# Optimization experiments

Measured on AMD Instinct MI355X. Metric: run time of the kernel, lower is better.

## Reference

```python
import jax, jax.numpy as jnp
import numpy as np

N, E, IN_FEATS, HID, CLS, K = 100000, 3200000, 500, 64, 40, 10
EPS = 1e-8

def _col_normalize(x):
    # column-wise L2 norm over nodes (dim=0), clamped at 1e-8
    return x / jnp.clip(jnp.linalg.norm(x, axis=0), EPS, None)

def setup_inputs() -> dict:
    key = jax.random.key(0)
    ks = jax.random.split(key, 9)
    features = jax.random.normal(ks[0], (N, IN_FEATS), jnp.float32)
    noise = jax.random.normal(ks[1], (N, HID), jnp.float32)
    edge_index = jax.random.randint(ks[2], (2, E), 0, N, dtype=jnp.int32)
    norm_A = jax.random.uniform(ks[3], (E,), jnp.float32) * 0.1  # normalized adj weights
    W1 = jax.random.normal(ks[4], (IN_FEATS, HID), jnp.float32) * (1.0 / np.sqrt(IN_FEATS))
    b1 = jax.random.normal(ks[5], (HID,), jnp.float32) * 0.01
    W2 = jax.random.normal(ks[6], (HID, CLS), jnp.float32) * (1.0 / np.sqrt(HID))
    b2 = jax.random.normal(ks[7], (CLS,), jnp.float32) * 0.01
    alpha = jax.random.normal(ks[8], (HID, K + 1), jnp.float32) * 0.1
    return {"features": features, "noise": noise, "norm_A": norm_A, "W1": W1,
            "b1": b1, "W2": W2, "b2": b2, "alpha": alpha, "edge_index": edge_index}

def reference(features, noise, norm_A, W1, b1, W2, b2, alpha, edge_index):
    # fc1 + act (dropout p=0 -> identity)
    x = jax.nn.relu(features @ W1 + b1)
    x = x + noise * 1e-5  # blank_noise = randn_like(x) * 1e-5
    h0 = _col_normalize(x)
    rst = alpha[:, 0] * h0  # broadcast per-channel over nodes
    last_h = h0
    second_last_h = jnp.zeros_like(h0)
    src, dst = edge_index[0], edge_index[1]
    for i in range(1, K + 1):
        # NormalBasisConv: h = A @ last_h (sparse), orthogonalize vs last two, column-normalize
        h = jax.ops.segment_sum(norm_A[:, None] * last_h[src], dst, num_segments=N)  # [N, HID]
        h = h - jnp.sum(h * last_h, axis=0) * last_h
        h = h - jnp.sum(h * second_last_h, axis=0) * second_last_h
        h = _col_normalize(h)
        rst = rst + alpha[:, i] * h
        second_last_h, last_h = last_h, h
    return rst @ W2 + b2
```

## Files before the change

### kernel.cpp

```cpp
#include <hip/hip_runtime.h>
#include <stdint.h>

#define N_NODES 100000
#define N_EDGES 3200000
#define IN_FEATS 500
#define HID 64
#define CLS 40
#define KHOPS 10
#define KT 32
#define NRANGE 8
#define SCAN_BS 256
#define SCAN_NBLK 391

__global__ void zero_kernel(float4* __restrict__ p, size_t n4) {
  size_t i = (size_t)blockIdx.x * blockDim.x + threadIdx.x;
  size_t stride = (size_t)gridDim.x * blockDim.x;
  float4 z = make_float4(0.f, 0.f, 0.f, 0.f);
  for (; i < n4; i += stride) p[i] = z;
}

__global__ void hist_kernel(const int* __restrict__ dst, int* __restrict__ off) {
  const int r = blockIdx.x & (NRANGE - 1);
  const int slice = blockIdx.x >> 3;
  const int nslices = gridDim.x >> 3;
  const int lo = r * (N_NODES / NRANGE);
  const int hi = lo + (N_NODES / NRANGE);
  const int per = (N_EDGES + nslices - 1) / nslices;
  const int beg = slice * per;
  int end = beg + per; if (end > N_EDGES) end = N_EDGES;
  for (int e = beg + threadIdx.x; e < end; e += blockDim.x) {
    int d = dst[e];
    if (d >= lo && d < hi) atomicAdd(&off[d + 1], 1);
  }
}

__launch_bounds__(SCAN_BS)
__global__ void scanA_kernel(const int* __restrict__ off, int* __restrict__ psum) {
  __shared__ int s[SCAN_BS];
  int b = blockIdx.x, t = threadIdx.x;
  int idx = b * SCAN_BS + t;
  s[t] = (idx < N_NODES + 1) ? off[idx] : 0;
  __syncthreads();
  for (int d = SCAN_BS / 2; d > 0; d >>= 1) {
    if (t < d) s[t] += s[t + d];
    __syncthreads();
  }
  if (t == 0) psum[b] = s[0];
}

__launch_bounds__(512)
__global__ void scanB_kernel(int* __restrict__ psum) {
  __shared__ int s[512];
  int t = threadIdx.x;
  s[t] = (t < SCAN_NBLK) ? psum[t] : 0;
  __syncthreads();
  for (int d = 1; d < 512; d <<= 1) {
    int v = (t >= d) ? s[t - d] : 0;
    __syncthreads();
    s[t] += v;
    __syncthreads();
  }
  if (t < SCAN_NBLK) psum[t] = (t == 0) ? 0 : s[t - 1];
}

__launch_bounds__(SCAN_BS)
__global__ void scanC_kernel(int* __restrict__ off, int* __restrict__ cursor,
                             const int* __restrict__ psum) {
  __shared__ int s[SCAN_BS];
  int b = blockIdx.x, t = threadIdx.x;
  int idx = b * SCAN_BS + t;
  s[t] = (idx < N_NODES + 1) ? off[idx] : 0;
  __syncthreads();
  for (int d = 1; d < SCAN_BS; d <<= 1) {
    int v = (t >= d) ? s[t - d] : 0;
    __syncthreads();
    s[t] += v;
    __syncthreads();
  }
  int run = s[t] + psum[b];
  if (idx < N_NODES + 1) {
    off[idx] = run;
    if (idx < N_NODES) cursor[idx] = run;
  }
}

__global__ void fill_kernel(const int* __restrict__ src, const int* __restrict__ dst,
                            const float* __restrict__ w, int* __restrict__ cursor,
                            int2* __restrict__ edges) {
  const int r = blockIdx.x & (NRANGE - 1);
  const int slice = blockIdx.x >> 3;
  const int nslices = gridDim.x >> 3;
  const int lo = r * (N_NODES / NRANGE);
  const int hi = lo + (N_NODES / NRANGE);
  const int per = (N_EDGES + nslices - 1) / nslices;
  const int beg = slice * per;
  int end = beg + per; if (end > N_EDGES) end = N_EDGES;
  for (int e = beg + threadIdx.x; e < end; e += blockDim.x) {
    int d = dst[e];
    if (d >= lo && d < hi) {
      int p = atomicAdd(&cursor[d], 1);
      edges[p] = make_int2(src[e], __float_as_int(w[e]));
    }
  }
}

__launch_bounds__(256)
__global__ void fc1_kernel(const float* __restrict__ F, const float* __restrict__ W1,
                           const float* __restrict__ bias1, const float* __restrict__ noise,
                           float* __restrict__ x, float* __restrict__ nn0) {
  __shared__ float Fs[KT][132];
  __shared__ float Ws[KT][64];
  __shared__ float red[64];
  const int t = threadIdx.x;
  const int tx = t & 15;
  const int ty = t >> 4;
  const int c0 = tx * 4;
  const int n0 = ty * 8;
  const int nodeBase = blockIdx.x * 128;
  const int fk = (t & 7) * 4;
  const int fn = t >> 3;
  const int wr = t >> 3;
  const int wc = (t & 7) * 8;

  float4 fr[4];
  float4 w0r, w1r;
  {
#pragma unroll
    for (int p = 0; p < 4; ++p) {
      int n = nodeBase + fn + 32 * p;
      float4 v = make_float4(0.f, 0.f, 0.f, 0.f);
      if (n < N_NODES && fk + 3 < IN_FEATS) v = *(const float4*)(F + (size_t)n * IN_FEATS + fk);
      fr[p] = v;
    }
    float4 a = make_float4(0.f, 0.f, 0.f, 0.f), b = a;
    if (wr < IN_FEATS) {
      a = *(const float4*)(W1 + (size_t)wr * HID + wc);
      b = *(const float4*)(W1 + (size_t)wr * HID + wc + 4);
    }
    w0r = a; w1r = b;
  }

  float acc[8][4];
#pragma unroll
  for (int i = 0; i < 8; ++i)
#pragma unroll
    for (int j = 0; j < 4; ++j) acc[i][j] = 0.f;

  const int NTILE = (IN_FEATS + KT - 1) / KT;
  for (int tile = 0; tile < NTILE; ++tile) {
    __syncthreads();
#pragma unroll
    for (int p = 0; p < 4; ++p) {
      Fs[fk + 0][fn + 32 * p] = fr[p].x;
      Fs[fk + 1][fn + 32 * p] = fr[p].y;
      Fs[fk + 2][fn + 32 * p] = fr[p].z;
      Fs[fk + 3][fn + 32 * p] = fr[p].w;
    }
    *(float4*)&Ws[wr][wc] = w0r;
    *(float4*)&Ws[wr][wc + 4] = w1r;
    __syncthreads();
    if (tile + 1 < NTILE) {
      const int kb = (tile + 1) * KT;
#pragma unroll
      for (int p = 0; p < 4; ++p) {
        int n = nodeBase + fn + 32 * p;
        int k = kb + fk;
        float4 v = make_float4(0.f, 0.f, 0.f, 0.f);
        if (n < N_NODES && k + 3 < IN_FEATS) v = *(const float4*)(F + (size_t)n * IN_FEATS + k);
        fr[p] = v;
      }
      int k = kb + wr;
      float4 a = make_float4(0.f, 0.f, 0.f, 0.f), b = a;
      if (k < IN_FEATS) {
        a = *(const float4*)(W1 + (size_t)k * HID + wc);
        b = *(const float4*)(W1 + (size_t)k * HID + wc + 4);
      }
      w0r = a; w1r = b;
    }
#pragma unroll 8
    for (int kk = 0; kk < KT; ++kk) {
      float4 fa = *(float4*)&Fs[kk][n0];
      float4 fb = *(float4*)&Fs[kk][n0 + 4];
      float4 wv = *(float4*)&Ws[kk][c0];
      acc[0][0] = fmaf(fa.x, wv.x, acc[0][0]); acc[0][1] = fmaf(fa.x, wv.y, acc[0][1]);
      acc[0][2] = fmaf(fa.x, wv.z, acc[0][2]); acc[0][3] = fmaf(fa.x, wv.w, acc[0][3]);
      acc[1][0] = fmaf(fa.y, wv.x, acc[1][0]); acc[1][1] = fmaf(fa.y, wv.y, acc[1][1]);
      acc[1][2] = fmaf(fa.y, wv.z, acc[1][2]); acc[1][3] = fmaf(fa.y, wv.w, acc[1][3]);
      acc[2][0] = fmaf(fa.z, wv.x, acc[2][0]); acc[2][1] = fmaf(fa.z, wv.y, acc[2][1]);
      acc[2][2] = fmaf(fa.z, wv.z, acc[2][2]); acc[2][3] = fmaf(fa.z, wv.w, acc[2][3]);
      acc[3][0] = fmaf(fa.w, wv.x, acc[3][0]); acc[3][1] = fmaf(fa.w, wv.y, acc[3][1]);
      acc[3][2] = fmaf(fa.w, wv.z, acc[3][2]); acc[3][3] = fmaf(fa.w, wv.w, acc[3][3]);
      acc[4][0] = fmaf(fb.x, wv.x, acc[4][0]); acc[4][1] = fmaf(fb.x, wv.y, acc[4][1]);
      acc[4][2] = fmaf(fb.x, wv.z, acc[4][2]); acc[4][3] = fmaf(fb.x, wv.w, acc[4][3]);
      acc[5][0] = fmaf(fb.y, wv.x, acc[5][0]); acc[5][1] = fmaf(fb.y, wv.y, acc[5][1]);
      acc[5][2] = fmaf(fb.y, wv.z, acc[5][2]); acc[5][3] = fmaf(fb.y, wv.w, acc[5][3]);
      acc[6][0] = fmaf(fb.z, wv.x, acc[6][0]); acc[6][1] = fmaf(fb.z, wv.y, acc[6][1]);
      acc[6][2] = fmaf(fb.z, wv.z, acc[6][2]); acc[6][3] = fmaf(fb.z, wv.w, acc[6][3]);
      acc[7][0] = fmaf(fb.w, wv.x, acc[7][0]); acc[7][1] = fmaf(fb.w, wv.y, acc[7][1]);
      acc[7][2] = fmaf(fb.w, wv.z, acc[7][2]); acc[7][3] = fmaf(fb.w, wv.w, acc[7][3]);
    }
  }

  float4 bb = *(const float4*)(bias1 + c0);
  float np0 = 0.f, np1 = 0.f, np2 = 0.f, np3 = 0.f;
#pragma unroll
  for (int i = 0; i < 8; ++i) {
    int n = nodeBase + n0 + i;
    if (n < N_NODES) {
      float4 nz = *(const float4*)(noise + (size_t)n * HID + c0);
      float v0 = fmaxf(acc[i][0] + bb.x, 0.f) + nz.x * 1e-5f;
      float v1 = fmaxf(acc[i][1] + bb.y, 0.f) + nz.y * 1e-5f;
      float v2 = fmaxf(acc[i][2] + bb.z, 0.f) + nz.z * 1e-5f;
      float v3 = fmaxf(acc[i][3] + bb.w, 0.f) + nz.w * 1e-5f;
      *(float4*)(x + (size_t)n * HID + c0) = make_float4(v0, v1, v2, v3);
      np0 = fmaf(v0, v0, np0); np1 = fmaf(v1, v1, np1);
      np2 = fmaf(v2, v2, np2); np3 = fmaf(v3, v3, np3);
    }
  }
  if (t < 64) red[t] = 0.f;
  __syncthreads();
  atomicAdd(&red[c0 + 0], np0); atomicAdd(&red[c0 + 1], np1);
  atomicAdd(&red[c0 + 2], np2); atomicAdd(&red[c0 + 3], np3);
  __syncthreads();
  if (t < 64) atomicAdd(&nn0[t], red[t]);
}

__launch_bounds__(256)
__global__ void spmm_kernel(const int2* __restrict__ edges, const int* __restrict__ off,
                            const float* __restrict__ lastr, const float* __restrict__ secondr,
                            const float* __restrict__ nn_l,
                            float* __restrict__ h, float* __restrict__ dslot) {
  __shared__ float red[128];
  const int t = threadIdx.x;
  const int lane = t & 63;
  const int wid = __builtin_amdgcn_readfirstlane(t >> 6);
  if (t < 128) red[t] = 0.f;
  __syncthreads();
  const float sig = 1.f / fmaxf(sqrtf(nn_l[lane]), 1e-8f);
  float d1 = 0.f, d2 = 0.f;
  const int nw = gridDim.x * 4;
  for (int n = blockIdx.x * 4 + wid; n < N_NODES; n += nw) {
    const int beg = off[n], end = off[n + 1];
    float a0 = 0.f, a1 = 0.f, a2 = 0.f, a3 = 0.f;
    float a4 = 0.f, a5 = 0.f, a6 = 0.f, a7 = 0.f;
    int j = beg;
    for (; j + 8 <= end; j += 8) {
      int2 e0 = edges[j + 0]; int2 e1 = edges[j + 1];
      int2 e2 = edges[j + 2]; int2 e3 = edges[j + 3];
      int2 e4 = edges[j + 4]; int2 e5 = edges[j + 5];
      int2 e6 = edges[j + 6]; int2 e7 = edges[j + 7];
      a0 = fmaf(__int_as_float(e0.y), lastr[(size_t)e0.x * HID + lane], a0);
      a1 = fmaf(__int_as_float(e1.y), lastr[(size_t)e1.x * HID + lane], a1);
      a2 = fmaf(__int_as_float(e2.y), lastr[(size_t)e2.x * HID + lane], a2);
      a3 = fmaf(__int_as_float(e3.y), lastr[(size_t)e3.x * HID + lane], a3);
      a4 = fmaf(__int_as_float(e4.y), lastr[(size_t)e4.x * HID + lane], a4);
      a5 = fmaf(__int_as_float(e5.y), lastr[(size_t)e5.x * HID + lane], a5);
      a6 = fmaf(__int_as_float(e6.y), lastr[(size_t)e6.x * HID + lane], a6);
      a7 = fmaf(__int_as_float(e7.y), lastr[(size_t)e7.x * HID + lane], a7);
    }
    for (; j < end; ++j) {
      int2 e = edges[j];
      a0 = fmaf(__int_as_float(e.y), lastr[(size_t)e.x * HID + lane], a0);
    }
    float acc = ((a0 + a1) + (a2 + a3)) + ((a4 + a5) + (a6 + a7));
    acc *= sig;
    size_t o = (size_t)n * HID + lane;
    float l = lastr[o], s = secondr[o];
    h[o] = acc;
    d1 = fmaf(acc, l, d1);
    d2 = fmaf(acc, s, d2);
  }
  atomicAdd(&red[lane], d1);
  atomicAdd(&red[64 + lane], d2);
  __syncthreads();
  if (t < 128) atomicAdd(&dslot[t], red[t]);
}

__launch_bounds__(256)
__global__ void passB_kernel(float4* __restrict__ h4, const float4* __restrict__ l4,
                             const float4* __restrict__ s4, float* __restrict__ dcur,
                             const float* __restrict__ nn_l, const float* __restrict__ nn_s,
                             const float* __restrict__ alpha, int prevcol, int accum,
                             float4* __restrict__ rst4) {
  __shared__ float red[64];
  int t = threadIdx.x;
  int q = t & 15;
  int c0 = q * 4;
  float4 NL = ((const float4*)nn_l)[q];
  float4 NS = ((const float4*)nn_s)[q];
  float4 D1 = ((const float4*)dcur)[q];
  float4 D2 = ((const float4*)(dcur + 64))[q];
  float4 sigl, sigs;
  sigl.x = 1.f / fmaxf(sqrtf(NL.x), 1e-8f); sigl.y = 1.f / fmaxf(sqrtf(NL.y), 1e-8f);
  sigl.z = 1.f / fmaxf(sqrtf(NL.z), 1e-8f); sigl.w = 1.f / fmaxf(sqrtf(NL.w), 1e-8f);
  sigs.x = 1.f / fmaxf(sqrtf(NS.x), 1e-8f); sigs.y = 1.f / fmaxf(sqrtf(NS.y), 1e-8f);
  sigs.z = 1.f / fmaxf(sqrtf(NS.z), 1e-8f); sigs.w = 1.f / fmaxf(sqrtf(NS.w), 1e-8f);
  float4 C1, C2, AL;
  C1.x = sigl.x * sigl.x * D1.x; C1.y = sigl.y * sigl.y * D1.y;
  C1.z = sigl.z * sigl.z * D1.z; C1.w = sigl.w * sigl.w * D1.w;
  C2.x = sigs.x * sigs.x * D2.x; C2.y = sigs.y * sigs.y * D2.y;
  C2.z = sigs.z * sigs.z * D2.z; C2.w = sigs.w * sigs.w * D2.w;
  AL.x = alpha[(size_t)(c0 + 0) * (KHOPS + 1) + prevcol] * sigl.x;
  AL.y = alpha[(size_t)(c0 + 1) * (KHOPS + 1) + prevcol] * sigl.y;
  AL.z = alpha[(size_t)(c0 + 2) * (KHOPS + 1) + prevcol] * sigl.z;
  AL.w = alpha[(size_t)(c0 + 3) * (KHOPS + 1) + prevcol] * sigl.w;
  float nx = 0.f, ny = 0.f, nz = 0.f, nw = 0.f;
  int row0 = blockIdx.x * 16 + (t >> 4);
  int rstride = gridDim.x * 16;
  for (int n = row0; n < N_NODES; n += rstride) {
    size_t idx = (size_t)n * 16 + q;
    float4 h = h4[idx];
    float4 l = l4[idx];
    float4 s = s4[idx];
    h.x -= C1.x * l.x + C2.x * s.x;
    h.y -= C1.y * l.y + C2.y * s.y;
    h.z -= C1.z * l.z + C2.z * s.z;
    h.w -= C1.w * l.w + C2.w * s.w;
    h4[idx] = h;
    nx = fmaf(h.x, h.x, nx); ny = fmaf(h.y, h.y, ny);
    nz = fmaf(h.z, h.z, nz); nw = fmaf(h.w, h.w, nw);
    float4 r;
    if (accum) {
      r = rst4[idx];
      r.x = fmaf(AL.x, l.x, r.x); r.y = fmaf(AL.y, l.y, r.y);
      r.z = fmaf(AL.z, l.z, r.z); r.w = fmaf(AL.w, l.w, r.w);
    } else {
      r.x = AL.x * l.x; r.y = AL.y * l.y; r.z = AL.z * l.z; r.w = AL.w * l.w;
    }
    rst4[idx] = r;
  }
  if (t < 64) red[t] = 0.f;
  __syncthreads();
  atomicAdd(&red[c0 + 0], nx); atomicAdd(&red[c0 + 1], ny);
  atomicAdd(&red[c0 + 2], nz); atomicAdd(&red[c0 + 3], nw);
  __syncthreads();
  if (t < 64) atomicAdd(&dcur[128 + t], red[t]);
}

__launch_bounds__(256)
__global__ void gemm2_kernel(const float* __restrict__ rst, const float* __restrict__ hK,
                             const float* __restrict__ nnK, const float* __restrict__ alpha,
                             const float* __restrict__ W2, const float* __restrict__ bias2,
                             float* __restrict__ out) {
  __shared__ float W2s[HID * CLS];
  __shared__ float R[64][65];
  __shared__ float coef[64];
  int t = threadIdx.x;
  if (t < 64) coef[t] = alpha[(size_t)t * (KHOPS + 1) + KHOPS] / fmaxf(sqrtf(nnK[t]), 1e-8f);
  for (int i = t; i < HID * CLS; i += 256) W2s[i] = W2[i];
  int nodeBase = blockIdx.x * 64;
  __syncthreads();
  for (int i = t; i < 64 * 16; i += 256) {
    int r = i >> 4, c4 = (i & 15) * 4;
    int n = nodeBase + r;
    if (n < N_NODES) {
      float4 rv = *(const float4*)(rst + (size_t)n * HID + c4);
      float4 hv = *(const float4*)(hK + (size_t)n * HID + c4);
      R[r][c4 + 0] = rv.x + coef[c4 + 0] * hv.x;
      R[r][c4 + 1] = rv.y + coef[c4 + 1] * hv.y;
      R[r][c4 + 2] = rv.z + coef[c4 + 2] * hv.z;
      R[r][c4 + 3] = rv.w + coef[c4 + 3] * hv.w;
    } else {
      R[r][c4 + 0] = 0.f; R[r][c4 + 1] = 0.f; R[r][c4 + 2] = 0.f; R[r][c4 + 3] = 0.f;
    }
  }
  __syncthreads();
  int node = t >> 2;
  int cls0 = (t & 3) * 10;
  float o[10];
#pragma unroll
  for (int j = 0; j < 10; ++j) o[j] = bias2[cls0 + j];
#pragma unroll 4
  for (int k = 0; k < HID; ++k) {
    float rv = R[node][k];
    const float* wrow = &W2s[k * CLS + cls0];
#pragma unroll
    for (int j = 0; j < 10; ++j) o[j] = fmaf(rv, wrow[j], o[j]);
  }
  int n = nodeBase + node;
  if (n < N_NODES) {
#pragma unroll
    for (int j = 0; j < 10; ++j) out[(size_t)n * CLS + cls0 + j] = o[j];
  }
}

extern "C" void kernel_launch(void* const* d_in, const int* in_sizes, int n_in,
                              void* d_out, int out_size, void* d_ws, size_t ws_size,
                              hipStream_t stream) {
  (void)in_sizes; (void)n_in; (void)out_size;
  const float* features  = (const float*)d_in[0];
  const float* noise     = (const float*)d_in[1];
  const float* norm_A    = (const float*)d_in[2];
  const float* W1        = (const float*)d_in[3];
  const float* b1        = (const float*)d_in[4];
  const float* W2        = (const float*)d_in[5];
  const float* b2        = (const float*)d_in[6];
  const float* alpha     = (const float*)d_in[7];
  const int*   edge_index= (const int*)d_in[8];
  float* out = (float*)d_out;

  char* ws = (char*)d_ws;
  const size_t NB = (size_t)N_NODES * HID * sizeof(float);
  const size_t CURSOR_PAD = 400128;
  float* hA    = (float*)(ws);
  float* hC    = (float*)(ws + NB);
  float* rst   = (float*)(ws + 2 * NB);
  int2*  edges = (int2*)(ws + 3 * NB);
  int*   cursor= (int*)(ws + 4 * NB);
  char*  zbase = ws + 4 * NB + CURSOR_PAD;
  float* hB    = (float*)(zbase);
  int*   off   = (int*)(zbase + NB);
  float* dots  = (float*)(zbase + NB + 400128);
  const size_t zspan = NB + 400128 + (size_t)12 * 192 * 4;
  int*   psum  = (int*)(zbase + zspan);
  const size_t total = 4 * NB + CURSOR_PAD + zspan + 4096;
  if (ws_size < total) return;

  zero_kernel<<<4096, 256, 0, stream>>>((float4*)zbase, zspan / 16);
  hist_kernel<<<2048, 256, 0, stream>>>(edge_index + N_EDGES, off);
  scanA_kernel<<<SCAN_NBLK, SCAN_BS, 0, stream>>>(off, psum);
  scanB_kernel<<<1, 512, 0, stream>>>(psum);
  scanC_kernel<<<SCAN_NBLK, SCAN_BS, 0, stream>>>(off, cursor, psum);
  fill_kernel<<<2048, 256, 0, stream>>>(edge_index, edge_index + N_EDGES, norm_A, cursor, edges);
  fc1_kernel<<<(N_NODES + 127) / 128, 256, 0, stream>>>(features, W1, b1, noise, hA,
                                                        dots + 1 * 192 + 128);
  float* second = hB; float* last = hA; float* cur = hC;
  for (int i = 1; i <= KHOPS; ++i) {
    float* dc = dots + (size_t)(i + 1) * 192;
    float* nl = dots + (size_t)(i)     * 192 + 128;
    float* ns = dots + (size_t)(i - 1) * 192 + 128;
    spmm_kernel<<<2048, 256, 0, stream>>>(edges, off, last, second, nl, cur, dc);
    passB_kernel<<<1024, 256, 0, stream>>>((float4*)cur, (const float4*)last,
                                           (const float4*)second, dc, nl, ns,
                                           alpha, i - 1, (i > 1) ? 1 : 0, (float4*)rst);
    float* tmp = second; second = last; last = cur; cur = tmp;
  }
  gemm2_kernel<<<(N_NODES + 63) / 64, 256, 0, stream>>>(rst, last,
                                                        dots + (size_t)(KHOPS + 1) * 192 + 128,
                                                        alpha, W2, b2, out);
}
```

Baseline: 2.636 ms.

## Split node features into 8-channel planes for cache-friendly SpMM gathers

Changes the feature layout from row-major [N,64] to eight planes of [N,8]. SpMM now processes one plane per block group, so each wavefront handles 8 edges at once with 8 lanes per edge and reduces with shuffles. The per-plane working set (3.2 MB) can fit in cache, which should cut DRAM traffic from the random gathers. Non-temporal loads are also added for the edge streams. In exchange, each edge list is read 8 times and only 8 of the 64 lanes are active in the epilogue. The launch grid must match the new blockIdx plane decoding, which happens in host code that is not shown.

After: 5.667 ms. +114.9%, slower.

```diff
diff --git a/kernel.cpp b/kernel.cpp
--- a/kernel.cpp
+++ b/kernel.cpp
@@ -11,6 +11,10 @@
 #define NRANGE 8
 #define SCAN_BS 256
 #define SCAN_NBLK 391
+#define PLN 8
+#define NPLANES 8
+#define PLSZ ((size_t)N_NODES * PLN)
+
 
 __global__ void zero_kernel(float4* __restrict__ p, size_t n4) {
   size_t i = (size_t)blockIdx.x * blockDim.x + threadIdx.x;
@@ -29,7 +33,7 @@
   const int beg = slice * per;
   int end = beg + per; if (end > N_EDGES) end = N_EDGES;
   for (int e = beg + threadIdx.x; e < end; e += blockDim.x) {
-    int d = dst[e];
+    int d = __builtin_nontemporal_load(dst + e);
     if (d >= lo && d < hi) atomicAdd(&off[d + 1], 1);
   }
 }
@@ -96,10 +100,12 @@
   const int beg = slice * per;
   int end = beg + per; if (end > N_EDGES) end = N_EDGES;
   for (int e = beg + threadIdx.x; e < end; e += blockDim.x) {
-    int d = dst[e];
+    int d = __builtin_nontemporal_load(dst + e);
     if (d >= lo && d < hi) {
+      int sv = __builtin_nontemporal_load(src + e);
+      float wv = __builtin_nontemporal_load(w + e);
       int p = atomicAdd(&cursor[d], 1);
-      edges[p] = make_int2(src[e], __float_as_int(w[e]));
+      edges[p] = make_int2(sv, __float_as_int(wv));
     }
   }
 }
@@ -121,6 +127,7 @@
   const int fn = t >> 3;
   const int wr = t >> 3;
   const int wc = (t & 7) * 8;
+  const size_t xplane = (size_t)(c0 >> 3) * PLSZ + (size_t)(c0 & 7);
 
   float4 fr[4];
   float4 w0r, w1r;
@@ -212,7 +219,7 @@
       float v1 = fmaxf(acc[i][1] + bb.y, 0.f) + nz.y * 1e-5f;
       float v2 = fmaxf(acc[i][2] + bb.z, 0.f) + nz.z * 1e-5f;
       float v3 = fmaxf(acc[i][3] + bb.w, 0.f) + nz.w * 1e-5f;
-      *(float4*)(x + (size_t)n * HID + c0) = make_float4(v0, v1, v2, v3);
+      *(float4*)(x + xplane + (size_t)n * 8) = make_float4(v0, v1, v2, v3);
       np0 = fmaf(v0, v0, np0); np1 = fmaf(v1, v1, np1);
       np2 = fmaf(v2, v2, np2); np3 = fmaf(v3, v3, np3);
     }
@@ -234,44 +241,53 @@
   const int t = threadIdx.x;
   const int lane = t & 63;
   const int wid = __builtin_amdgcn_readfirstlane(t >> 6);
+  const int p = __builtin_amdgcn_readfirstlane(blockIdx.x >> 8);
+  const int pb = blockIdx.x & 255;
+  const int c = lane & 7;
+  const int g = lane >> 3;
   if (t < 128) red[t] = 0.f;
   __syncthreads();
-  const float sig = 1.f / fmaxf(sqrtf(nn_l[lane]), 1e-8f);
+  const float* __restrict__ pl = lastr + (size_t)p * PLSZ;
+  const float* __restrict__ ps = secondr + (size_t)p * PLSZ;
+  float* __restrict__ ph = h + (size_t)p * PLSZ;
+  const float sig = 1.f / fmaxf(sqrtf(nn_l[p * PLN + c]), 1e-8f);
+  const long long* __restrict__ eL = (const long long*)edges;
   float d1 = 0.f, d2 = 0.f;
-  const int nw = gridDim.x * 4;
-  for (int n = blockIdx.x * 4 + wid; n < N_NODES; n += nw) {
+  for (int n = pb * 4 + wid; n < N_NODES; n += 1024) {
     const int beg = off[n], end = off[n + 1];
-    float a0 = 0.f, a1 = 0.f, a2 = 0.f, a3 = 0.f;
-    float a4 = 0.f, a5 = 0.f, a6 = 0.f, a7 = 0.f;
+    float a0 = 0.f, a1 = 0.f;
     int j = beg;
-    for (; j + 8 <= end; j += 8) {
-      int2 e0 = edges[j + 0]; int2 e1 = edges[j + 1];
-      int2 e2 = edges[j + 2]; int2 e3 = edges[j + 3];
-      int2 e4 = edges[j + 4]; int2 e5 = edges[j + 5];
-      int2 e6 = edges[j + 6]; int2 e7 = edges[j + 7];
-      a0 = fmaf(__int_as_float(e0.y), lastr[(size_t)e0.x * HID + lane], a0);
-      a1 = fmaf(__int_as_float(e1.y), lastr[(size_t)e1.x * HID + lane], a1);
-      a2 = fmaf(__int_as_float(e2.y), lastr[(size_t)e2.x * HID + lane], a2);
-      a3 = fmaf(__int_as_float(e3.y), lastr[(size_t)e3.x * HID + lane], a3);
-      a4 = fmaf(__int_as_float(e4.y), lastr[(size_t)e4.x * HID + lane], a4);
-      a5 = fmaf(__int_as_float(e5.y), lastr[(size_t)e5.x * HID + lane], a5);
-      a6 = fmaf(__int_as_float(e6.y), lastr[(size_t)e6.x * HID + lane], a6);
-      a7 = fmaf(__int_as_float(e7.y), lastr[(size_t)e7.x * HID + lane], a7);
-    }
-    for (; j < end; ++j) {
-      int2 e = edges[j];
-      a0 = fmaf(__int_as_float(e.y), lastr[(size_t)e.x * HID + lane], a0);
-    }
-    float acc = ((a0 + a1) + (a2 + a3)) + ((a4 + a5) + (a6 + a7));
+    for (; j + 16 <= end; j += 16) {
+      long long e0 = __builtin_nontemporal_load(eL + j + g);
+      long long e1 = __builtin_nontemporal_load(eL + j + 8 + g);
+      a0 = fmaf(__int_as_float((int)(e0 >> 32)), pl[(size_t)(int)e0 * PLN + c], a0);
+      a1 = fmaf(__int_as_float((int)(e1 >> 32)), pl[(size_t)(int)e1 * PLN + c], a1);
+    }
+    for (; j < end; j += 8) {
+      int idx = j + g;
+      int ci = idx < end ? idx : end - 1;
+      long long e = __builtin_nontemporal_load(eL + ci);
+      float w = (idx < end) ? __int_as_float((int)(e >> 32)) : 0.f;
+      a0 = fmaf(w, pl[(size_t)(int)e * PLN + c], a0);
+    }
+    float acc = a0 + a1;
+    acc += __shfl_xor(acc, 8);
+    acc += __shfl_xor(acc, 16);
+    acc += __shfl_xor(acc, 32);
     acc *= sig;
-    size_t o = (size_t)n * HID + lane;
-    float l = lastr[o], s = secondr[o];
-    h[o] = acc;
-    d1 = fmaf(acc, l, d1);
-    d2 = fmaf(acc, s, d2);
-  }
-  atomicAdd(&red[lane], d1);
-  atomicAdd(&red[64 + lane], d2);
+    if (lane < 8) {
+      size_t o = (size_t)n * PLN + c;
+      float l = pl[o];
+      float s = __builtin_nontemporal_load(ps + o);
+      __builtin_nontemporal_store(acc, ph + o);
+      d1 = fmaf(acc, l, d1);
+      d2 = fmaf(acc, s, d2);
+    }
+  }
+  if (lane < 8) {
+    atomicAdd(&red[p * PLN + c], d1);
+    atomicAdd(&red[64 + p * PLN + c], d2);
+  }
   __syncthreads();
   if (t < 128) atomicAdd(&dslot[t], red[t]);
 }
@@ -283,56 +299,61 @@
                              const float* __restrict__ alpha, int prevcol, int accum,
                              float4* __restrict__ rst4) {
   __shared__ float red[64];
-  int t = threadIdx.x;
-  int q = t & 15;
-  int c0 = q * 4;
-  float4 NL = ((const float4*)nn_l)[q];
-  float4 NS = ((const float4*)nn_s)[q];
-  float4 D1 = ((const float4*)dcur)[q];
-  float4 D2 = ((const float4*)(dcur + 64))[q];
-  float4 sigl, sigs;
-  sigl.x = 1.f / fmaxf(sqrtf(NL.x), 1e-8f); sigl.y = 1.f / fmaxf(sqrtf(NL.y), 1e-8f);
-  sigl.z = 1.f / fmaxf(sqrtf(NL.z), 1e-8f); sigl.w = 1.f / fmaxf(sqrtf(NL.w), 1e-8f);
-  sigs.x = 1.f / fmaxf(sqrtf(NS.x), 1e-8f); sigs.y = 1.f / fmaxf(sqrtf(NS.y), 1e-8f);
-  sigs.z = 1.f / fmaxf(sqrtf(NS.z), 1e-8f); sigs.w = 1.f / fmaxf(sqrtf(NS.w), 1e-8f);
-  float4 C1, C2, AL;
-  C1.x = sigl.x * sigl.x * D1.x; C1.y = sigl.y * sigl.y * D1.y;
-  C1.z = sigl.z * sigl.z * D1.z; C1.w = sigl.w * sigl.w * D1.w;
-  C2.x = sigs.x * sigs.x * D2.x; C2.y = sigs.y * sigs.y * D2.y;
-  C2.z = sigs.z * sigs.z * D2.z; C2.w = sigs.w * sigs.w * D2.w;
-  AL.x = alpha[(size_t)(c0 + 0) * (KHOPS + 1) + prevcol] * sigl.x;
-  AL.y = alpha[(size_t)(c0 + 1) * (KHOPS + 1) + prevcol] * sigl.y;
-  AL.z = alpha[(size_t)(c0 + 2) * (KHOPS + 1) + prevcol] * sigl.z;
-  AL.w = alpha[(size_t)(c0 + 3) * (KHOPS + 1) + prevcol] * sigl.w;
-  float nx = 0.f, ny = 0.f, nz = 0.f, nw = 0.f;
-  int row0 = blockIdx.x * 16 + (t >> 4);
-  int rstride = gridDim.x * 16;
-  for (int n = row0; n < N_NODES; n += rstride) {
-    size_t idx = (size_t)n * 16 + q;
-    float4 h = h4[idx];
-    float4 l = l4[idx];
-    float4 s = s4[idx];
-    h.x -= C1.x * l.x + C2.x * s.x;
-    h.y -= C1.y * l.y + C2.y * s.y;
-    h.z -= C1.z * l.z + C2.z * s.z;
-    h.w -= C1.w * l.w + C2.w * s.w;
-    h4[idx] = h;
-    nx = fmaf(h.x, h.x, nx); ny = fmaf(h.y, h.y, ny);
-    nz = fmaf(h.z, h.z, nz); nw = fmaf(h.w, h.w, nw);
-    float4 r;
-    if (accum) {
-      r = rst4[idx];
-      r.x = fmaf(AL.x, l.x, r.x); r.y = fmaf(AL.y, l.y, r.y);
-      r.z = fmaf(AL.z, l.z, r.z); r.w = fmaf(AL.w, l.w, r.w);
-    } else {
-      r.x = AL.x * l.x; r.y = AL.y * l.y; r.z = AL.z * l.z; r.w = AL.w * l.w;
-    }
-    rst4[idx] = r;
-  }
+  const int t = threadIdx.x;
   if (t < 64) red[t] = 0.f;
   __syncthreads();
-  atomicAdd(&red[c0 + 0], nx); atomicAdd(&red[c0 + 1], ny);
-  atomicAdd(&red[c0 + 2], nz); atomicAdd(&red[c0 + 3], nw);
+  const int half = t & 1;
+  const size_t stride = (size_t)gridDim.x * blockDim.x;
+  const size_t f0 = (size_t)blockIdx.x * blockDim.x + t;
+  const size_t NP4 = (size_t)N_NODES * 2;
+#pragma unroll 1
+  for (int p = 0; p < NPLANES; ++p) {
+    const int cb = p * PLN + half * 4;
+    float4 NL = *(const float4*)(nn_l + cb);
+    float4 NS = *(const float4*)(nn_s + cb);
+    float4 D1 = *(const float4*)(dcur + cb);
+    float4 D2 = *(const float4*)(dcur + 64 + cb);
+    float4 sigl, sigs;
+    sigl.x = 1.f / fmaxf(sqrtf(NL.x), 1e-8f); sigl.y = 1.f / fmaxf(sqrtf(NL.y), 1e-8f);
+    sigl.z = 1.f / fmaxf(sqrtf(NL.z), 1e-8f); sigl.w = 1.f / fmaxf(sqrtf(NL.w), 1e-8f);
+    sigs.x = 1.f / fmaxf(sqrtf(NS.x), 1e-8f); sigs.y = 1.f / fmaxf(sqrtf(NS.y), 1e-8f);
+    sigs.z = 1.f / fmaxf(sqrtf(NS.z), 1e-8f); sigs.w = 1.f / fmaxf(sqrtf(NS.w), 1e-8f);
+    float4 C1, C2, AL;
+    C1.x = sigl.x * sigl.x * D1.x; C1.y = sigl.y * sigl.y * D1.y;
+    C1.z = sigl.z * sigl.z * D1.z; C1.w = sigl.w * sigl.w * D1.w;
+    C2.x = sigs.x * sigs.x * D2.x; C2.y = sigs.y * sigs.y * D2.y;
+    C2.z = sigs.z * sigs.z * D2.z; C2.w = sigs.w * sigs.w * D2.w;
+    AL.x = alpha[(size_t)(cb + 0) * (KHOPS + 1) + prevcol] * sigl.x;
+    AL.y = alpha[(size_t)(cb + 1) * (KHOPS + 1) + prevcol] * sigl.y;
+    AL.z = alpha[(size_t)(cb + 2) * (KHOPS + 1) + prevcol] * sigl.z;
+    AL.w = alpha[(size_t)(cb + 3) * (KHOPS + 1) + prevcol] * sigl.w;
+    const size_t pb = (size_t)p * NP4;
+    float nx = 0.f, ny = 0.f, nz = 0.f, nw = 0.f;
+    for (size_t f = f0; f < NP4; f += stride) {
+      size_t idx = pb + f;
+      float4 h = h4[idx];
+      float4 l = l4[idx];
+      float4 s = s4[idx];
+      h.x -= C1.x * l.x + C2.x * s.x;
+      h.y -= C1.y * l.y + C2.y * s.y;
+      h.z -= C1.z * l.z + C2.z * s.z;
+      h.w -= C1.w * l.w + C2.w * s.w;
+      h4[idx] = h;
+      nx = fmaf(h.x, h.x, nx); ny = fmaf(h.y, h.y, ny);
+      nz = fmaf(h.z, h.z, nz); nw = fmaf(h.w, h.w, nw);
+      float4 r;
+      if (accum) {
+        r = rst4[idx];
+        r.x = fmaf(AL.x, l.x, r.x); r.y = fmaf(AL.y, l.y, r.y);
+        r.z = fmaf(AL.z, l.z, r.z); r.w = fmaf(AL.w, l.w, r.w);
+      } else {
+        r.x = AL.x * l.x; r.y = AL.y * l.y; r.z = AL.z * l.z; r.w = AL.w * l.w;
+      }
+      rst4[idx] = r;
+    }
+    atomicAdd(&red[cb + 0], nx); atomicAdd(&red[cb + 1], ny);
+    atomicAdd(&red[cb + 2], nz); atomicAdd(&red[cb + 3], nw);
+  }
   __syncthreads();
   if (t < 64) atomicAdd(&dcur[128 + t], red[t]);
 }
@@ -351,17 +372,19 @@
   int nodeBase = blockIdx.x * 64;
   __syncthreads();
   for (int i = t; i < 64 * 16; i += 256) {
-    int r = i >> 4, c4 = (i & 15) * 4;
+    int r = i >> 4, grp = i & 15;
+    int cb = grp * 4;
     int n = nodeBase + r;
+    size_t idx = (size_t)(grp >> 1) * PLSZ + (size_t)n * 8 + (grp & 1) * 4;
     if (n < N_NODES) {
-      float4 rv = *(const float4*)(rst + (size_t)n * HID + c4);
-      float4 hv = *(const float4*)(hK + (size_t)n * HID + c4);
-      R[r][c4 + 0] = rv.x + coef[c4 + 0] * hv.x;
-      R[r][c4 + 1] = rv.y + coef[c4 + 1] * hv.y;
-      R[r][c4 + 2] = rv.z + coef[c4 + 2] * hv.z;
-      R[r][c4 + 3] = rv.w + coef[c4 + 3] * hv.w;
+      float4 rv = *(const float4*)(rst + idx);
+      float4 hv = *(const float4*)(hK + idx);
+      R[r][cb + 0] = rv.x + coef[cb + 0] * hv.x;
+      R[r][cb + 1] = rv.y + coef[cb + 1] * hv.y;
+      R[r][cb + 2] = rv.z + coef[cb + 2] * hv.z;
+      R[r][cb + 3] = rv.w + coef[cb + 3] * hv.w;
     } else {
-      R[r][c4 + 0] = 0.f; R[r][c4 + 1] = 0.f; R[r][c4 + 2] = 0.f; R[r][c4 + 3] = 0.f;
+      R[r][cb + 0] = 0.f; R[r][cb + 1] = 0.f; R[r][cb + 2] = 0.f; R[r][cb + 3] = 0.f;
     }
   }
   __syncthreads();
```
